# Kernel optimization log

Hardware: AMD Instinct MI355X
Metric: run time of the kernel (lower is better)

Reference implementation:

```python
import jax, jax.numpy as jnp
import numpy as np

D = 1024
H = 1024
N = 64
T = 512


def setup_inputs() -> dict:
    key = jax.random.key(0)
    k1, k2, k3, k4 = jax.random.split(key, 4)
    x = jax.random.normal(k1, (N, T, D), dtype=jnp.float32)
    h0 = jax.random.normal(k2, (N, H), dtype=jnp.float32)
    Wx = jax.random.normal(k3, (D, 4 * H), dtype=jnp.float32) / np.sqrt(D)
    Wh = jax.random.normal(k4, (H, 4 * H), dtype=jnp.float32) / np.sqrt(H)
    b = jnp.zeros((4 * H,), dtype=jnp.float32)
    return {"x": x, "h0": h0, "Wx": Wx, "Wh": Wh, "b": b}


def _lstm(x, h0, Wx, Wh, b):
    # Precompute input contribution for all timesteps in one big GEMM:
    # xW: (T, N, 4H)
    xW = jnp.einsum('ntd,dk->tnk', x, Wx) + b
    c0 = jnp.zeros_like(h0)
    Hdim = h0.shape[1]

    def step(carry, xw_t):
        prev_h, prev_c = carry
        a = xw_t + prev_h @ Wh  # (N, 4H)
        i = jax.nn.sigmoid(a[:, 0:Hdim])
        f = jax.nn.sigmoid(a[:, Hdim:2 * Hdim])
        o = jax.nn.sigmoid(a[:, 2 * Hdim:3 * Hdim])
        g = jnp.tanh(a[:, 3 * Hdim:4 * Hdim])
        next_c = f * prev_c + i * g
        next_h = o * jnp.tanh(next_c)
        return (next_h, next_c), next_h

    _, hs = jax.lax.scan(step, (h0, c0), xW)  # hs: (T, N, H)
    return jnp.transpose(hs, (1, 0, 2))  # (N, T, H)


def reference(x, h0, Wx, Wh, b):
    return _lstm(x, h0, Wx, Wh, b)
```

## Files before the change

kernel.cpp:

```cpp
#include <hip/hip_runtime.h>
#include <hip/hip_bf16.h>
#include <hip/hip_cooperative_groups.h>
#include <cstdio>

namespace cg = cooperative_groups;

#define NBATCH 64
#define TSTEPS 512
#define DDIM   1024
#define HDIM   1024
#define ACOLS  4096
#define NBLK   256
#define NTHR   256
#define HCB    4
#define KPX    1032

typedef __attribute__((ext_vector_type(8))) short bf16x8;
typedef __attribute__((ext_vector_type(4))) float f32x4;
typedef unsigned int  u32;
typedef unsigned short u16;
typedef unsigned long long u64;

__device__ __forceinline__ u16 bf_hi(float f) { __hip_bfloat16 h = __float2bfloat16(f); return *(u16*)&h; }
__device__ __forceinline__ float bf2f(u16 u)  { __hip_bfloat16 h = *(__hip_bfloat16*)&u; return __bfloat162float(h); }


__global__ __launch_bounds__(NTHR, 1)
void lstm_kernel(const float* __restrict__ xf,
                 const float* __restrict__ h0,
                 const float* __restrict__ Wx,
                 const float* __restrict__ Wh,
                 const float* __restrict__ bias,
                 float* __restrict__ out,
                 u16* __restrict__ x_hi,
                 u16* __restrict__ x_lo,
                 u32* __restrict__ hslot,
                 u32* __restrict__ flags)
{
  extern __shared__ char smem[];
  short* sWxh = (short*)smem;
  short* sWxl = sWxh + 16 * KPX;
  short* sWhh = sWxl + 16 * KPX;
  short* sWhl = sWhh + 16 * KPX;
  float* accb   = (float*)(sWhl + 16 * KPX);
  float* hstage = accb + 64 * 17;

  const int blk  = blockIdx.x;
  const int tid  = threadIdx.x;
  const int lane = tid & 63;
  const int wave = tid >> 6;
  const int gid  = blk * NTHR + tid;
  cg::grid_group grid = cg::this_grid();

  {
    const long NX = (long)NBATCH * TSTEPS * DDIM;
    for (long i = (long)gid * 4; i < NX; i += (long)NBLK * NTHR * 4) {
      const float4 v = *(const float4*)(xf + i);
      ushort4 hi, lo;
      hi.x = bf_hi(v.x); lo.x = bf_hi(v.x - bf2f(hi.x));
      hi.y = bf_hi(v.y); lo.y = bf_hi(v.y - bf2f(hi.y));
      hi.z = bf_hi(v.z); lo.z = bf_hi(v.z - bf2f(hi.z));
      hi.w = bf_hi(v.w); lo.w = bf_hi(v.w - bf2f(hi.w));
      *(ushort4*)(x_hi + i) = hi;
      *(ushort4*)(x_lo + i) = lo;
    }
    for (int i = gid; i < NBATCH * HDIM; i += NBLK * NTHR) {
      const int n = i >> 10, k = i & 1023;
      const int w = n >> 4, r = n & 15, c = k >> 5, q = (k >> 3) & 3, j = k & 7;
      ((u16*)hslot)[(w * 32 + c) * 512 + 128 * q + 8 * r + j] = bf_hi(h0[i]);
    }
    if (gid < NBLK)
      __hip_atomic_store(&flags[gid], 0u, __ATOMIC_RELAXED, __HIP_MEMORY_SCOPE_AGENT);
  }

  for (int it = tid; it < DDIM * 4; it += NTHR) {
    const int k = it & 1023, g = it >> 10;
    const float4 wx = *(const float4*)(Wx + (size_t)k * ACOLS + g * HDIM + blk * HCB);
    const float4 wh = *(const float4*)(Wh + (size_t)k * ACOLS + g * HDIM + blk * HCB);
    const float* wxp = &wx.x;
    const float* whp = &wh.x;
    #pragma unroll
    for (int j = 0; j < 4; ++j) {
      const int col = g * 4 + j;
      const u16 xh = bf_hi(wxp[j]);
      sWxh[col * KPX + k] = (short)xh;
      sWxl[col * KPX + k] = (short)bf_hi(wxp[j] - bf2f(xh));
      const u16 hh = bf_hi(whp[j]);
      sWhh[col * KPX + k] = (short)hh;
      sWhl[col * KPX + k] = (short)bf_hi(whp[j] - bf2f(hh));
    }
  }

  const int gn = tid >> 2;
  const int ghc = tid & 3;
  float bb[4];
  #pragma unroll
  for (int g = 0; g < 4; ++g) bb[g] = bias[g * HDIM + blk * HCB + ghc];
  float cst = 0.0f;

  int hw_q = 0;
  {
    const int k0 = blk * HCB;
    const int w2 = tid >> 4, r2 = tid & 15, c2 = k0 >> 5, q2 = (k0 >> 3) & 3, j0 = k0 & 7;
    hw_q = ((w2 * 32 + c2) * 256 + 64 * q2 + 4 * r2 + (j0 >> 1)) >> 1;
  }

  const int mrow = lane & 15;
  const int kq   = lane >> 4;
  const int n0   = wave * 16 + mrow;
  const u16* xh_row = x_hi + (size_t)n0 * (TSTEPS * DDIM) + 8 * kq;
  const u16* xl_row = x_lo + (size_t)n0 * (TSTEPS * DDIM) + 8 * kq;
  const short* bxh = sWxh + mrow * KPX + 8 * kq;
  const short* bxl = sWxl + mrow * KPX + 8 * kq;
  const short* bhh = sWhh + mrow * KPX + 8 * kq;
  const short* bhl = sWhl + mrow * KPX + 8 * kq;

  auto xgemm = [&](int s) -> f32x4 {
    const u16* xh_p = xh_row + (size_t)s * DDIM;
    const u16* xl_p = xl_row + (size_t)s * DDIM;
    f32x4 a = {0.f, 0.f, 0.f, 0.f};
    bf16x8 Ah[4], Al[4], Bh[4], Bl[4];
    #pragma unroll
    for (int p = 0; p < 4; ++p) {
      Ah[p] = *(const bf16x8*)(xh_p + p * 32);
      Al[p] = *(const bf16x8*)(xl_p + p * 32);
      Bh[p] = *(const bf16x8*)(bxh + p * 32);
      Bl[p] = *(const bf16x8*)(bxl + p * 32);
    }
    #pragma unroll
    for (int i = 0; i < 32; ++i) {
      const int sl = i & 3;
      a = __builtin_amdgcn_mfma_f32_16x16x32_bf16(Ah[sl], Bh[sl], a, 0, 0, 0);
      a = __builtin_amdgcn_mfma_f32_16x16x32_bf16(Ah[sl], Bl[sl], a, 0, 0, 0);
      a = __builtin_amdgcn_mfma_f32_16x16x32_bf16(Al[sl], Bh[sl], a, 0, 0, 0);
      if (i < 28) {
        Ah[sl] = *(const bf16x8*)(xh_p + (i + 4) * 32);
        Al[sl] = *(const bf16x8*)(xl_p + (i + 4) * 32);
        Bh[sl] = *(const bf16x8*)(bxh + (i + 4) * 32);
        Bl[sl] = *(const bf16x8*)(bxl + (i + 4) * 32);
      }
    }
    return a;
  };

  grid.sync();

  f32x4 acc_x = xgemm(0);

  for (int s = 0; s < TSTEPS; ++s) {
    if (s > 0) {
      if (wave == 0) {
        const uint4* fp = reinterpret_cast<const uint4*>(flags) + lane;
        for (;;) {
          uint4 f;
          asm volatile("global_load_dwordx4 %0, %1, off sc0 sc1\n\ts_waitcnt vmcnt(0)"
                       : "=v"(f) : "v"(fp) : "memory");
          const bool ok = (f.x >= (u32)s) & (f.y >= (u32)s) & (f.z >= (u32)s) & (f.w >= (u32)s);
          if (__all(ok)) break;
          __builtin_amdgcn_s_sleep(2);
        }
      }
      __syncthreads();
    }

    f32x4 acc = acc_x;
    {
      u32* hsrc = hslot + (size_t)(s & 1) * 32768;
      const uint4* hb = (const uint4*)(hsrc + 4 * lane);
      union AU { uint4 u; bf16x8 v; };
      AU A[32];
      #pragma unroll
      for (int p = 0; p < 32; ++p) {
        const uint4* hp = hb + (wave * 32 + p) * 64;
        asm volatile("global_load_dwordx4 %0, %1, off sc0 sc1"
                     : "=v"(A[p].u) : "v"(hp));
      }
      asm volatile("s_waitcnt vmcnt(0)" ::: "memory");
      __builtin_amdgcn_sched_barrier(0);
      #pragma unroll
      for (int i = 0; i < 32; ++i) {
        acc = __builtin_amdgcn_mfma_f32_16x16x32_bf16(A[i].v, *(const bf16x8*)(bhh + i * 32), acc, 0, 0, 0);
        acc = __builtin_amdgcn_mfma_f32_16x16x32_bf16(A[i].v, *(const bf16x8*)(bhl + i * 32), acc, 0, 0, 0);
      }
    }

    #pragma unroll
    for (int r = 0; r < 4; ++r)
      accb[(wave * 16 + kq * 4 + r) * 17 + mrow] = acc[r];
    __syncthreads();

    float hv;
    {
      float av[4];
      #pragma unroll
      for (int g = 0; g < 4; ++g) av[g] = accb[gn * 17 + g * 4 + ghc] + bb[g];
      const float ig = 1.0f / (1.0f + __expf(-av[0]));
      const float fg = 1.0f / (1.0f + __expf(-av[1]));
      const float og = 1.0f / (1.0f + __expf(-av[2]));
      const float e2 = __expf(2.0f * av[3]);
      const float gg = (e2 - 1.0f) / (e2 + 1.0f);
      cst = fg * cst + ig * gg;
      const float e2c = __expf(2.0f * cst);
      hv = og * ((e2c - 1.0f) / (e2c + 1.0f));
      hstage[gn * 4 + ghc] = hv;
    }
    __syncthreads();

    if (tid < 64) {
      const float4 h4 = *(const float4*)(hstage + tid * 4);
      const u32 p0 = (u32)bf_hi(h4.x) | ((u32)bf_hi(h4.y) << 16);
      const u32 p1 = (u32)bf_hi(h4.z) | ((u32)bf_hi(h4.w) << 16);
      const u64 pk = (u64)p0 | ((u64)p1 << 32);
      u64* hdst = (u64*)(hslot + (size_t)((s + 1) & 1) * 32768) + hw_q;
      __hip_atomic_store(hdst, pk, __ATOMIC_RELAXED, __HIP_MEMORY_SCOPE_AGENT);
    }
    asm volatile("s_waitcnt vmcnt(0)" ::: "memory");
    __syncthreads();
    if (tid == 0)
      __hip_atomic_store(&flags[blk], (u32)(s + 1), __ATOMIC_RELAXED, __HIP_MEMORY_SCOPE_AGENT);

    out[(size_t)gn * (TSTEPS * HDIM) + (size_t)s * HDIM + blk * HCB + ghc] = hv;
    if (s + 1 < TSTEPS)
      acc_x = xgemm(s + 1);
  }
}

extern "C" void kernel_launch(void* const* d_in, const int* in_sizes, int n_in,
                              void* d_out, int out_size, void* d_ws, size_t ws_size,
                              hipStream_t stream) {
  const float* x  = (const float*)d_in[0];
  const float* h0 = (const float*)d_in[1];
  const float* Wx = (const float*)d_in[2];
  const float* Wh = (const float*)d_in[3];
  const float* b  = (const float*)d_in[4];
  float* out = (float*)d_out;

  const size_t XPL = (size_t)NBATCH * TSTEPS * DDIM * 2;
  u16* x_hi  = (u16*)d_ws;
  u16* x_lo  = (u16*)((char*)d_ws + XPL);
  u32* hslot = (u32*)((char*)d_ws + 2 * XPL);
  u32* flags = (u32*)((char*)d_ws + 2 * XPL + 2 * 65536 * 2);

  const size_t smem = (size_t)(4 * 16 * KPX * 2) + (64 * 17 + 64 * 4) * sizeof(float);
  hipError_t e1 = hipFuncSetAttribute((const void*)lstm_kernel,
                                      hipFuncAttributeMaxDynamicSharedMemorySize, (int)smem);

  void* args[] = { (void*)&x, (void*)&h0, (void*)&Wx, (void*)&Wh, (void*)&b,
                   (void*)&out, (void*)&x_hi, (void*)&x_lo, (void*)&hslot, (void*)&flags };
  hipError_t e2 = hipLaunchCooperativeKernel((const void*)lstm_kernel, dim3(NBLK), dim3(NTHR),
                                             args, (unsigned)smem, stream);
  if (e1 != hipSuccess || e2 != hipSuccess)
    fprintf(stderr, "[lstm] setattr=%d launch=%d (%s)\n", (int)e1, (int)e2, hipGetErrorString(e2));
}
```

Before: 9.722 ms.

## Warp-specialize blocks: dedicated waves precompute next-step x-GEMM via LDS ring

Blocks grow from 4 to 8 waves. Waves 0-3 run the recurrent h@Wh MFMA at raised priority, while waves 4-7 compute the input projection for the next timestep concurrently and store it in a two-slot LDS ring. Before, the x-GEMM ran serially after each step's flag publish, so it sat partly on the critical path. In exchange the block uses more threads and LDS, and the flag spin loop is now bounded, so a slow peer could let a block proceed with stale h.

```diff
diff --git a/kernel.cpp b/kernel.cpp
--- a/kernel.cpp
+++ b/kernel.cpp
@@ -11,9 +11,11 @@
 #define HDIM   1024
 #define ACOLS  4096
 #define NBLK   256
-#define NTHR   256
+#define NTHR   512
 #define HCB    4
 #define KPX    1032
+#define RING   2
+#define LEAD   1
 
 typedef __attribute__((ext_vector_type(8))) short bf16x8;
 typedef __attribute__((ext_vector_type(4))) float f32x4;
@@ -25,7 +27,7 @@
 __device__ __forceinline__ float bf2f(u16 u)  { __hip_bfloat16 h = *(__hip_bfloat16*)&u; return __bfloat162float(h); }
 
 
-__global__ __launch_bounds__(NTHR, 1)
+__global__ __launch_bounds__(NTHR, 2)
 void lstm_kernel(const float* __restrict__ xf,
                  const float* __restrict__ h0,
                  const float* __restrict__ Wx,
@@ -44,6 +46,7 @@
   short* sWhl = sWhh + 16 * KPX;
   float* accb   = (float*)(sWhl + 16 * KPX);
   float* hstage = accb + 64 * 17;
+  float* ringf  = hstage + 64 * 4;
 
   const int blk  = blockIdx.x;
   const int tid  = threadIdx.x;
@@ -107,17 +110,14 @@
 
   const int mrow = lane & 15;
   const int kq   = lane >> 4;
-  const int n0   = wave * 16 + mrow;
-  const u16* xh_row = x_hi + (size_t)n0 * (TSTEPS * DDIM) + 8 * kq;
-  const u16* xl_row = x_lo + (size_t)n0 * (TSTEPS * DDIM) + 8 * kq;
   const short* bxh = sWxh + mrow * KPX + 8 * kq;
   const short* bxl = sWxl + mrow * KPX + 8 * kq;
   const short* bhh = sWhh + mrow * KPX + 8 * kq;
   const short* bhl = sWhl + mrow * KPX + 8 * kq;
 
-  auto xgemm = [&](int s) -> f32x4 {
-    const u16* xh_p = xh_row + (size_t)s * DDIM;
-    const u16* xl_p = xl_row + (size_t)s * DDIM;
+  auto xgemm_rg = [&](int s, int rg) {
+    const u16* xh_p = x_hi + (size_t)(rg * 16 + mrow) * (TSTEPS * DDIM) + (size_t)s * DDIM + 8 * kq;
+    const u16* xl_p = x_lo + (size_t)(rg * 16 + mrow) * (TSTEPS * DDIM) + (size_t)s * DDIM + 8 * kq;
     f32x4 a = {0.f, 0.f, 0.f, 0.f};
     bf16x8 Ah[4], Al[4], Bh[4], Bl[4];
     #pragma unroll
@@ -140,18 +140,23 @@
         Bl[sl] = *(const bf16x8*)(bxl + (i + 4) * 32);
       }
     }
-    return a;
+    const int slot = s & (RING - 1);
+    #pragma unroll
+    for (int r = 0; r < 4; ++r)
+      ringf[(slot * 64 + rg * 16 + kq * 4 + r) * 17 + mrow] = a[r];
   };
 
   grid.sync();
 
-  f32x4 acc_x = xgemm(0);
+  if (wave < 4)
+    xgemm_rg(0, wave);
+  __syncthreads();
 
   for (int s = 0; s < TSTEPS; ++s) {
     if (s > 0) {
       if (wave == 0) {
         const uint4* fp = reinterpret_cast<const uint4*>(flags) + lane;
-        for (;;) {
+        for (int spin = 0; spin < (1 << 17); ++spin) {
           uint4 f;
           asm volatile("global_load_dwordx4 %0, %1, off sc0 sc1\n\ts_waitcnt vmcnt(0)"
                        : "=v"(f) : "v"(fp) : "memory");
@@ -163,34 +168,45 @@
       __syncthreads();
     }
 
-    f32x4 acc = acc_x;
-    {
-      u32* hsrc = hslot + (size_t)(s & 1) * 32768;
-      const uint4* hb = (const uint4*)(hsrc + 4 * lane);
-      union AU { uint4 u; bf16x8 v; };
-      AU A[32];
+    if (wave < 4) {
+      __builtin_amdgcn_s_setprio(1);
+      f32x4 acc;
+      {
+        const int sb = (s & (RING - 1)) * 64 + wave * 16 + kq * 4;
+        #pragma unroll
+        for (int r = 0; r < 4; ++r) acc[r] = ringf[(sb + r) * 17 + mrow];
+      }
+      {
+        u32* hsrc = hslot + (size_t)(s & 1) * 32768;
+        const uint4* hb = (const uint4*)(hsrc + 4 * lane);
+        union AU { uint4 u; bf16x8 v; };
+        AU A[32];
+        #pragma unroll
+        for (int p = 0; p < 32; ++p) {
+          const uint4* hp = hb + (wave * 32 + p) * 64;
+          asm volatile("global_load_dwordx4 %0, %1, off sc0 sc1"
+                       : "=v"(A[p].u) : "v"(hp));
+        }
+        asm volatile("s_waitcnt vmcnt(0)" ::: "memory");
+        __builtin_amdgcn_sched_barrier(0);
+        #pragma unroll
+        for (int i = 0; i < 32; ++i) {
+          acc = __builtin_amdgcn_mfma_f32_16x16x32_bf16(A[i].v, *(const bf16x8*)(bhh + i * 32), acc, 0, 0, 0);
+          acc = __builtin_amdgcn_mfma_f32_16x16x32_bf16(A[i].v, *(const bf16x8*)(bhl + i * 32), acc, 0, 0, 0);
+        }
+      }
       #pragma unroll
-      for (int p = 0; p < 32; ++p) {
-        const uint4* hp = hb + (wave * 32 + p) * 64;
-        asm volatile("global_load_dwordx4 %0, %1, off sc0 sc1"
-                     : "=v"(A[p].u) : "v"(hp));
-      }
-      asm volatile("s_waitcnt vmcnt(0)" ::: "memory");
-      __builtin_amdgcn_sched_barrier(0);
-      #pragma unroll
-      for (int i = 0; i < 32; ++i) {
-        acc = __builtin_amdgcn_mfma_f32_16x16x32_bf16(A[i].v, *(const bf16x8*)(bhh + i * 32), acc, 0, 0, 0);
-        acc = __builtin_amdgcn_mfma_f32_16x16x32_bf16(A[i].v, *(const bf16x8*)(bhl + i * 32), acc, 0, 0, 0);
-      }
-    }
-
-    #pragma unroll
-    for (int r = 0; r < 4; ++r)
-      accb[(wave * 16 + kq * 4 + r) * 17 + mrow] = acc[r];
+      for (int r = 0; r < 4; ++r)
+        accb[(wave * 16 + kq * 4 + r) * 17 + mrow] = acc[r];
+      __builtin_amdgcn_s_setprio(0);
+    } else {
+      if (s + LEAD < TSTEPS)
+        xgemm_rg(s + LEAD, wave - 4);
+    }
     __syncthreads();
 
-    float hv;
-    {
+    float hv = 0.0f;
+    if (tid < 256) {
       float av[4];
       #pragma unroll
       for (int g = 0; g < 4; ++g) av[g] = accb[gn * 17 + g * 4 + ghc] + bb[g];
@@ -218,10 +234,8 @@
     __syncthreads();
     if (tid == 0)
       __hip_atomic_store(&flags[blk], (u32)(s + 1), __ATOMIC_RELAXED, __HIP_MEMORY_SCOPE_AGENT);
-
-    out[(size_t)gn * (TSTEPS * HDIM) + (size_t)s * HDIM + blk * HCB + ghc] = hv;
-    if (s + 1 < TSTEPS)
-      acc_x = xgemm(s + 1);
+    if (tid < 256)
+      out[(size_t)gn * (TSTEPS * HDIM) + (size_t)s * HDIM + blk * HCB + ghc] = hv;
   }
 }
 
@@ -241,7 +255,8 @@
   u32* hslot = (u32*)((char*)d_ws + 2 * XPL);
   u32* flags = (u32*)((char*)d_ws + 2 * XPL + 2 * 65536 * 2);
 
-  const size_t smem = (size_t)(4 * 16 * KPX * 2) + (64 * 17 + 64 * 4) * sizeof(float);
+  const size_t smem = (size_t)(4 * 16 * KPX * 2)
+                    + (size_t)(64 * 17 + 64 * 4 + RING * 64 * 17) * sizeof(float);
   hipError_t e1 = hipFuncSetAttribute((const void*)lstm_kernel,
                                       hipFuncAttributeMaxDynamicSharedMemorySize, (int)smem);
 
```

Result: slower. 10.43 ms (+7.3%).
